# Kernel optimization log

Hardware: AMD Instinct MI355X
Metric: run time of the kernel (lower is better)

Reference implementation:

```python
import jax, jax.numpy as jnp
import numpy as np
from jax import lax

CHAR_H = 100
HIDDEN = 512
N_LABELS = 64
WORD_D = 300
CHAR_D = 50
FORGET_BIAS = 1.0
BN_EPS = 1e-3


def lstm(x, W, b, lens):
    """TF BasicLSTMCell dynamic_rnn. x:[B,T,D], W:[D+H,4H], b:[4H], lens:[B].
    Returns (outputs [B,T,H] zeroed past lens, (c,h) final states held at lens)."""
    B, T, _ = x.shape
    H = W.shape[1] // 4
    def step(carry, inp):
        c, h = carry
        xt, t = inp
        z = jnp.concatenate([xt, h], axis=-1) @ W + b
        i, j, f, o = jnp.split(z, 4, axis=-1)  # TF gate order i, j(g), f, o
        c_new = c * jax.nn.sigmoid(f + FORGET_BIAS) + jax.nn.sigmoid(i) * jnp.tanh(j)
        h_new = jnp.tanh(c_new) * jax.nn.sigmoid(o)
        active = (t < lens)[:, None]
        c = jnp.where(active, c_new, c)
        h = jnp.where(active, h_new, h)
        out = jnp.where(active, h_new, jnp.zeros_like(h_new))
        return (c, h), out
    init = (jnp.zeros((B, H), x.dtype), jnp.zeros((B, H), x.dtype))
    (c, h), outs = lax.scan(step, init, (jnp.swapaxes(x, 0, 1), jnp.arange(T)))
    return jnp.swapaxes(outs, 0, 1), (c, h)


def reverse_seq(x, lens):
    """tf.reverse_sequence along time axis 1."""
    T = x.shape[1]
    t = jnp.arange(T)[None, :]
    idx = jnp.where(t < lens[:, None], lens[:, None] - 1 - t, t)
    return jnp.take_along_axis(x, idx[:, :, None], axis=1)


def _glorot(key, shape):
    fan_in, fan_out = shape[0], shape[1]
    s = np.sqrt(6.0 / (fan_in + fan_out)).astype(np.float32)
    return jax.random.uniform(key, shape, jnp.float32, -s, s)


def setup_inputs() -> dict:
    key = jax.random.key(0)
    ks = jax.random.split(key, 16)
    N_SUB, SUB_T = 16384, 25
    B, T = 64, 256
    d_word_in = WORD_D + 2 * CHAR_H  # 500
    inp = {
        "subwords": jax.random.normal(ks[0], (N_SUB, SUB_T, CHAR_D), jnp.float32),
        "tokens": jax.random.normal(ks[1], (B, T, WORD_D), jnp.float32),
        "token_subword": jax.random.randint(ks[2], (B, T), 0, N_SUB, jnp.int32),
        "subword_seq_lens": jax.random.randint(ks[3], (N_SUB,), 1, SUB_T + 1, jnp.int32),
        "seq_lens": jax.random.randint(ks[4], (B,), 1, T + 1, jnp.int32),
        "Wc_f": _glorot(ks[5], (CHAR_D + CHAR_H, 4 * CHAR_H)),
        "bc_f": jnp.zeros((4 * CHAR_H,), jnp.float32),
        "Wc_b": _glorot(ks[6], (CHAR_D + CHAR_H, 4 * CHAR_H)),
        "bc_b": jnp.zeros((4 * CHAR_H,), jnp.float32),
        "Ww_f": _glorot(ks[7], (d_word_in + HIDDEN, 4 * HIDDEN)),
        "bw_f": jnp.zeros((4 * HIDDEN,), jnp.float32),
        "Ww_b": _glorot(ks[8], (d_word_in + HIDDEN, 4 * HIDDEN)),
        "bw_b": jnp.zeros((4 * HIDDEN,), jnp.float32),
        "Wo": _glorot(ks[9], (2 * HIDDEN + HIDDEN, 4 * HIDDEN)),
        "bo": jnp.zeros((4 * HIDDEN,), jnp.float32),
        "bn_gamma": jnp.ones((HIDDEN,), jnp.float32),
        "bn_beta": jnp.zeros((HIDDEN,), jnp.float32),
        "Wt": _glorot(ks[10], (HIDDEN, N_LABELS)),
        "bt": jnp.zeros((N_LABELS,), jnp.float32),
    }
    return inp


def reference(subwords, tokens, token_subword, subword_seq_lens, seq_lens,
              Wc_f, bc_f, Wc_b, bc_b, Ww_f, bw_f, Ww_b, bw_b,
              Wo, bo, bn_gamma, bn_beta, Wt, bt):
    # --- char/subword BiLSTM: only final hidden states are used ---
    _, (_, hf) = lstm(subwords, Wc_f, bc_f, subword_seq_lens)
    _, (_, hb) = lstm(reverse_seq(subwords, subword_seq_lens), Wc_b, bc_b, subword_seq_lens)
    subword_reprs = jnp.concatenate([hf, hb], axis=1)           # [N_sub, 200]
    tok_sub = subword_reprs[token_subword]                      # [B,T,200]
    word_in = jnp.concatenate([tokens, tok_sub], axis=2)        # [B,T,500]
    # --- word BiLSTM ---
    f_out, _ = lstm(word_in, Ww_f, bw_f, seq_lens)
    b_out_r, _ = lstm(reverse_seq(word_in, seq_lens), Ww_b, bw_b, seq_lens)
    b_out = reverse_seq(b_out_r, seq_lens)
    hidden = jnp.concatenate([f_out, b_out], axis=2)            # [B,T,1024]
    # --- top unidirectional LSTM ---
    out2, _ = lstm(hidden, Wo, bo, seq_lens)                    # [B,T,512]
    # --- batch norm over all but last dim (contrib.layers.batch_norm) ---
    mean = jnp.mean(out2, axis=(0, 1))
    var = jnp.var(out2, axis=(0, 1))
    bn = bn_gamma * (out2 - mean) * lax.rsqrt(var + BN_EPS) + bn_beta
    # --- tag affine ---
    logits = bn @ Wt + bt                                       # [B,T,n_labels]
    return logits
```

## Files before the change

### kernel.cpp

```cpp
#include <hip/hip_runtime.h>
#include <cstdint>
#include <cstddef>


typedef unsigned short bf_t;
typedef __attribute__((ext_vector_type(8))) short bf16x8;
typedef __attribute__((ext_vector_type(4))) float f32x4;

#define DEVI __device__ __forceinline__
DEVI float bf2f(bf_t u){ return __uint_as_float(((unsigned)u)<<16); }
DEVI bf_t  f2bf(float f){ unsigned u=__float_as_uint(f); return (bf_t)((u + 0x7FFFu + ((u>>16)&1u))>>16); }
DEVI float sigx(float x){ return __builtin_amdgcn_rcpf(1.0f + __builtin_amdgcn_exp2f(-1.44269504f*x)); }
DEVI float tanx(float x){ return 2.0f*__builtin_amdgcn_rcpf(1.0f + __builtin_amdgcn_exp2f(-2.88539008f*x)) - 1.0f; }

__global__ void k_dbg(float* out, unsigned mb){ out[0] = (float)mb; }

__global__ __launch_bounds__(256) void k_prep_charm(const float* __restrict__ wcf,
    const float* __restrict__ wcb, bf_t* __restrict__ wct){
  int i = blockIdx.x*256 + threadIdx.x;
  if (i >= 2*400*160) return;
  int kk = i % 160; int r = i / 160;
  int np = r % 400; int dir = r / 400;
  int u = np >> 2, g = np & 3;
  const float* w = dir ? wcb : wcf;
  wct[i] = (kk < 150) ? f2bf(w[kk*400 + g*100 + u]) : (bf_t)0;
}
__global__ __launch_bounds__(256) void k_prep_wrec(const float* __restrict__ wwf,
    const float* __restrict__ wwb, bf_t* __restrict__ wrg){
  int i = blockIdx.x*256 + threadIdx.x;
  if (i >= 2*2048*512) return;
  int k = i & 511; int np = (i >> 9) & 2047; int dir = i >> 20;
  int c = np >> 2, g = np & 3;
  const float* w = dir ? wwb : wwf;
  wrg[i] = f2bf(w[(size_t)(500 + k)*2048 + g*512 + c]);
}
__global__ __launch_bounds__(256) void k_prep_trec(const float* __restrict__ wo,
    bf_t* __restrict__ wog){
  int i = blockIdx.x*256 + threadIdx.x;
  if (i >= 2048*512) return;
  int k = i & 511; int np = i >> 9;
  int c = np >> 2, g = np & 3;
  wog[i] = f2bf(wo[(size_t)(1024 + k)*2048 + g*512 + c]);
}
__global__ __launch_bounds__(256) void k_prep_wx(const float* __restrict__ wwf,
    const float* __restrict__ wwb, bf_t* __restrict__ wx){
  int i = blockIdx.x*256 + threadIdx.x;
  if (i >= 2*2048*512) return;
  int k = i & 511; int r = i >> 9;
  int np = r & 2047; int dir = r >> 11;
  int c = np >> 2, g = np & 3;
  const float* w = dir ? wwb : wwf;
  wx[i] = (k < 500) ? f2bf(w[(size_t)k*2048 + g*512 + c]) : (bf_t)0;
}
__global__ __launch_bounds__(256) void k_prep_wxt(const float* __restrict__ wo,
    bf_t* __restrict__ wxt){
  int i = blockIdx.x*256 + threadIdx.x;
  if (i >= 2048*1024) return;
  int k = i & 1023; int np = i >> 10;
  int c = np >> 2, g = np & 3;
  wxt[i] = f2bf(wo[(size_t)k*2048 + g*512 + c]);
}
__global__ __launch_bounds__(256) void k_prep_bias(const float* __restrict__ bwf,
    const float* __restrict__ bwb, const float* __restrict__ bo,
    float* __restrict__ bpf, float* __restrict__ bpb, float* __restrict__ bpt){
  int np = blockIdx.x*256 + threadIdx.x;
  if (np >= 2048) return;
  int c = np >> 2, g = np & 3;
  bpf[np] = bwf[g*512 + c];
  bpb[np] = bwb[g*512 + c];
  bpt[np] = bo[g*512 + c];
}
__global__ __launch_bounds__(256) void k_ridx(const int* __restrict__ lens,
    int* __restrict__ ridxb){
  int b = blockIdx.x, t = threadIdx.x;
  int L = lens[b];
  int tin = (t < L) ? (L - 1 - t) : t;
  ridxb[b*256 + t] = b*256 + tin;
}

DEVI int aslot(int s, int kk){
  return (((kk >> 5)*4 + ((kk >> 3) & 3))*16 + s)*8 + (kk & 7);
}
__global__ __launch_bounds__(256) void k_charm(const float* __restrict__ subwords,
    const int* __restrict__ slens, const bf_t* __restrict__ wct,
    const float* __restrict__ bcf, const float* __restrict__ bcb,
    bf_t* __restrict__ rep){
  const int dir = blockIdx.y;
  const int s0 = blockIdx.x * 16;
  const int tid = threadIdx.x;
  const int w = tid >> 6, lane = tid & 63;
  const int l16 = lane & 15, lk = lane >> 4;

  __shared__ __align__(16) bf_t abuf[2560];
  __shared__ float zs[16][409];
  __shared__ float bs[400];
  __shared__ int lens[16];

  if (tid < 16) lens[tid] = slens[s0 + tid];
  for (int i = tid; i < 1280; i += 256) ((float*)abuf)[i] = 0.f;
  {
    const float* bc = dir ? bcb : bcf;
    for (int i = tid; i < 400; i += 256) bs[i] = bc[(i & 3)*100 + (i >> 2)];
  }
  __syncthreads();

  int si[4], ki[4], Lr[4]; bool vr[4];
#pragma unroll
  for (int r = 0; r < 4; r++) {
    int i = tid + r*256;
    vr[r] = (i < 800);
    si[r] = vr[r] ? (i / 50) : 0;
    ki[r] = vr[r] ? (i - si[r]*50) : 0;
    Lr[r] = lens[si[r]];
  }
  float pf[4];
  auto loadx = [&](int t){
#pragma unroll
    for (int r = 0; r < 4; r++) {
      if (vr[r]) {
        int te = dir ? (Lr[r] - 1 - t) : t;
        te = te < 0 ? 0 : te;
        pf[r] = subwords[((size_t)(s0 + si[r])*25 + te)*50 + ki[r]];
      }
    }
  };
  loadx(0);

  const bf_t* wctd = wct + (size_t)dir*400*160;
  float c7[7];
#pragma unroll
  for (int j = 0; j < 7; j++) c7[j] = 0.f;

  for (int t = 0; t < 25; t++) {
#pragma unroll
    for (int r = 0; r < 4; r++)
      if (vr[r]) abuf[aslot(si[r], ki[r])] = f2bf(pf[r]);
    __syncthreads();
    if (t < 24) loadx(t + 1);

    f32x4 acc[7];
#pragma unroll
    for (int jj = 0; jj < 7; jj++) acc[jj] = (f32x4){0.f,0.f,0.f,0.f};
#pragma unroll
    for (int ks = 0; ks < 5; ks++) {
      bf16x8 af = *(const bf16x8*)&abuf[((ks*4 + lk)*16 + l16)*8];
#pragma unroll
      for (int jj = 0; jj < 7; jj++) {
        int j = w + jj*4;
        if (j < 25) {
          bf16x8 bv = *(const bf16x8*)(wctd + (size_t)(j*16 + l16)*160 + ks*32 + lk*8);
          acc[jj] = __builtin_amdgcn_mfma_f32_16x16x32_bf16(af, bv, acc[jj], 0, 0, 0);
        }
      }
    }
#pragma unroll
    for (int jj = 0; jj < 7; jj++) {
      int j = w + jj*4;
      if (j < 25) {
#pragma unroll
        for (int r = 0; r < 4; r++)
          zs[lk*4 + r][j*16 + l16] = acc[jj][r];
      }
    }
    __syncthreads();

#pragma unroll
    for (int j = 0; j < 7; j++) {
      int idx = j*256 + tid;
      if (idx < 1600) {
        int s = idx & 15, u = idx >> 4;
        int L = lens[s];
        if (t < L) {
          float zi = zs[s][u*4 + 0] + bs[u*4 + 0];
          float zj = zs[s][u*4 + 1] + bs[u*4 + 1];
          float zf = zs[s][u*4 + 2] + bs[u*4 + 2];
          float zo = zs[s][u*4 + 3] + bs[u*4 + 3];
          float cn = c7[j]*sigx(zf + 1.0f) + sigx(zi)*tanx(zj);
          float hn = tanx(cn)*sigx(zo);
          c7[j] = cn;
          bf_t hb = f2bf(hn);
          abuf[aslot(s, 50 + u)] = hb;
          if (t == L - 1) rep[(size_t)(s0 + s)*200 + dir*100 + u] = hb;
        }
      }
    }
  }
}

__global__ __launch_bounds__(128) void k_win(const float* __restrict__ tokens,
    const bf_t* __restrict__ rep, const int* __restrict__ tsub,
    bf_t* __restrict__ win){
  int row = blockIdx.x;
  int idx = tsub[row];
  const float* tsrc = tokens + (size_t)row*300;
  const bf_t* rsrc = rep + (size_t)idx*200;
  bf_t* w = win + (size_t)row*512;
  for (int i = threadIdx.x; i < 512; i += 128)
    w[i] = (i < 300) ? f2bf(tsrc[i]) : (i < 500 ? rsrc[i - 300] : (bf_t)0);
}

__global__ __launch_bounds__(256) void k_mgemm(const bf_t* __restrict__ A, int lda, int K,
    const bf_t* __restrict__ B0, const bf_t* __restrict__ B1,
    const float* __restrict__ bp0, const float* __restrict__ bp1,
    bf_t* __restrict__ C0, bf_t* __restrict__ C1,
    const int* __restrict__ ridx1, int t0){
  const int z = blockIdx.z;
  const bf_t* B = z ? B1 : B0;
  const float* bp = z ? bp1 : bp0;
  bf_t* C = z ? C1 : C0;
  const int* ridx = z ? ridx1 : nullptr;
  __shared__ short As[4096];
  __shared__ short Bs[4096];
  const int tid = threadIdx.x;
  const int rb = blockIdx.y*128, nb = blockIdx.x*128;
  const bf_t* srcA[2]; const bf_t* srcB[2];
#pragma unroll
  for (int q = 0; q < 2; q++) {
    int s = tid + q*256;
    int row = ((s >> 6) << 4) + (s & 15), kg = (s >> 4) & 3;
    int lr = rb + row;
    int v = (t0 >= 0) ? ((lr >> 6)*256 + t0 + (lr & 63)) : lr;
    int ga = ridx ? ridx[v] : v;
    srcA[q] = A + (size_t)ga*lda + kg*8;
    srcB[q] = B + (size_t)(nb + row)*K + kg*8;
  }
  f32x4 acc[4][4];
#pragma unroll
  for (int i = 0; i < 4; i++)
#pragma unroll
    for (int j = 0; j < 4; j++) acc[i][j] = (f32x4){0.f,0.f,0.f,0.f};
  const int wid = tid >> 6, lane = tid & 63;
  const int wr = wid >> 1, wc = wid & 1;
  const int l16 = lane & 15, lk = lane >> 4;

  uint4 va0 = *(const uint4*)(srcA[0]);
  uint4 va1 = *(const uint4*)(srcA[1]);
  uint4 vb0 = *(const uint4*)(srcB[0]);
  uint4 vb1 = *(const uint4*)(srcB[1]);
  for (int kb = 0; kb < K; kb += 32) {
    __syncthreads();
    *(uint4*)&As[(size_t)tid*8] = va0;
    *(uint4*)&As[(size_t)(tid+256)*8] = va1;
    *(uint4*)&Bs[(size_t)tid*8] = vb0;
    *(uint4*)&Bs[(size_t)(tid+256)*8] = vb1;
    __syncthreads();
    if (kb + 32 < K) {
      va0 = *(const uint4*)(srcA[0] + kb + 32);
      va1 = *(const uint4*)(srcA[1] + kb + 32);
      vb0 = *(const uint4*)(srcB[0] + kb + 32);
      vb1 = *(const uint4*)(srcB[1] + kb + 32);
    }
    bf16x8 af[4], bfr[4];
#pragma unroll
    for (int f = 0; f < 4; f++) {
      af[f]  = *(const bf16x8*)&As[(((wr*4 + f)*4 + lk)*16 + l16)*8];
      bfr[f] = *(const bf16x8*)&Bs[(((wc*4 + f)*4 + lk)*16 + l16)*8];
    }
#pragma unroll
    for (int i = 0; i < 4; i++)
#pragma unroll
      for (int j = 0; j < 4; j++)
        acc[i][j] = __builtin_amdgcn_mfma_f32_16x16x32_bf16(af[i], bfr[j], acc[i][j], 0, 0, 0);
  }
#pragma unroll
  for (int i = 0; i < 4; i++) {
    int row0 = wr*64 + i*16 + lk*4;
#pragma unroll
    for (int j = 0; j < 4; j++) {
      int col = nb + wc*64 + j*16 + l16;
      float bv = bp[col];
#pragma unroll
      for (int r = 0; r < 4; r++)
        C[(size_t)(rb + row0 + r)*2048 + col] = f2bf(acc[i][j][r] + bv);
    }
  }
}

__global__ __launch_bounds__(512) void k_chunk(
    bf_t* __restrict__ hx0, bf_t* __restrict__ hx1,
    float* __restrict__ cst, const bf_t* __restrict__ wrec,
    const bf_t* __restrict__ zxf, const bf_t* __restrict__ zxb,
    const int* __restrict__ seq_lens, bf_t* __restrict__ outp,
    unsigned* __restrict__ ctrs, int t0, int is_top){
  const int dir = is_top ? 0 : blockIdx.y;
  const int n = blockIdx.x;
  const int npb = n*128;
  const unsigned nblk = gridDim.x;
  unsigned* ctr = ctrs + dir*32;
  const int tid = threadIdx.x;
  const int w = tid >> 6, lane = tid & 63;
  const int l16 = lane & 15, lk = lane >> 4;

  __shared__ __align__(16) char smem[65536];
  float (*zs)[132] = (float(*)[132])smem;

  const bf_t* B = wrec + ((size_t)dir*2048 + npb + w*16)*512;
  const bf_t* zx = (dir ? zxb : zxf);
  unsigned long long* hx08 = (unsigned long long*)hx0 + (size_t)dir*8192;
  unsigned long long* hx18 = (unsigned long long*)hx1 + (size_t)dir*8192;

  bf16x8 bfr[16];
#pragma unroll
  for (int ks = 0; ks < 16; ks++)
    bfr[ks] = *(const bf16x8*)(B + (size_t)l16*512 + ks*32 + lk*8);

  const int b = tid >> 3, q = tid & 7, u0 = q*4;
  const int len = seq_lens[b];
  const int cg0 = (npb >> 2) + u0;
  const size_t cbase = ((size_t)dir*64 + b)*512 + cg0;
  float creg[4];
#pragma unroll
  for (int it = 0; it < 4; it++) creg[it] = cst[cbase + it];
  const size_t hslot = (size_t)n*512 + b*8 + q;
  unsigned long long hpack = __hip_atomic_load(
      ((t0 & 1) ? hx18 : hx08) + hslot,
      __ATOMIC_RELAXED, __HIP_MEMORY_SCOPE_AGENT);

  for (int s = 0; s < 64; s++) {
    const int t = t0 + s;
    unsigned long long* hr8 = (t & 1) ? hx18 : hx08;
    unsigned long long* hw8 = (t & 1) ? hx08 : hx18;

    const int tl = t & 63;
    uint4 zq[2];
    {
      const char* zxp = (const char*)(zx + ((size_t)(b*64 + tl))*2048 + (size_t)(npb + u0*4));
      zq[0] = *(const uint4*)zxp;
      zq[1] = *(const uint4*)(zxp + 16);
    }

#pragma unroll
    for (int it = 0; it < 16; it++) {
      int i = it*512 + tid;
      int nn = i >> 9, r9 = i & 511;
      int bb = r9 >> 3, qq = r9 & 7;
      unsigned long long v = __hip_atomic_load(hr8 + i,
          __ATOMIC_RELAXED, __HIP_MEMORY_SCOPE_AGENT);
      int cb = nn*64 + qq*8;
      *(unsigned long long*)&smem[bb*1024 + (((cb & ~15) ^ ((bb & 7) << 4)) | (cb & 15))] = v;
    }
    __syncthreads();

    f32x4 acc[4];
#pragma unroll
    for (int mf = 0; mf < 4; mf++) acc[mf] = (f32x4){0.f,0.f,0.f,0.f};
#pragma unroll
    for (int ks = 0; ks < 16; ks++) {
#pragma unroll
      for (int mf = 0; mf < 4; mf++) {
        int row = mf*16 + l16;
        bf16x8 af = *(const bf16x8*)&smem[row*1024 + ((ks*64 + lk*16) ^ ((row & 7) << 4))];
        acc[mf] = __builtin_amdgcn_mfma_f32_16x16x32_bf16(af, bfr[ks], acc[mf], 0, 0, 0);
      }
    }
    __syncthreads();

#pragma unroll
    for (int mf = 0; mf < 4; mf++)
#pragma unroll
      for (int r = 0; r < 4; r++)
        zs[mf*16 + lk*4 + r][w*16 + l16] = acc[mf][r];
    __syncthreads();

    if (t < len) {
      const ushort* zu = (const ushort*)zq;
      bf_t hb4[4];
#pragma unroll
      for (int it = 0; it < 4; it++) {
        float zi = zs[b][(u0 + it)*4 + 0] + bf2f(zu[it*4 + 0]);
        float zj = zs[b][(u0 + it)*4 + 1] + bf2f(zu[it*4 + 1]);
        float zf = zs[b][(u0 + it)*4 + 2] + bf2f(zu[it*4 + 2]);
        float zo = zs[b][(u0 + it)*4 + 3] + bf2f(zu[it*4 + 3]);
        float cn = creg[it]*sigx(zf + 1.0f) + sigx(zi)*tanx(zj);
        float hn = tanx(cn)*sigx(zo);
        creg[it] = cn;
        hb4[it] = f2bf(hn);
      }
      hpack = *(unsigned long long*)hb4;
      if (is_top) {
        *(ushort4*)&outp[((size_t)b*256 + t)*512 + cg0] = *(ushort4*)hb4;
      } else {
        int tin = dir ? (len - 1 - t) : t;
        *(ushort4*)&outp[((size_t)b*256 + tin)*1024 + dir*512 + cg0] = *(ushort4*)hb4;
      }
    }
    __hip_atomic_store(hw8 + hslot, hpack,
                       __ATOMIC_RELAXED, __HIP_MEMORY_SCOPE_AGENT);

    __syncthreads();
    if (tid == 0) {
      __hip_atomic_fetch_add(ctr, 1u, __ATOMIC_RELAXED, __HIP_MEMORY_SCOPE_AGENT);
      unsigned tgt = (unsigned)(s + 1) * nblk;
      while (__hip_atomic_load(ctr, __ATOMIC_RELAXED, __HIP_MEMORY_SCOPE_AGENT) < tgt) {
        __builtin_amdgcn_s_sleep(1);
      }
    }
    __syncthreads();
  }
#pragma unroll
  for (int it = 0; it < 4; it++) cst[cbase + it] = creg[it];
}

__global__ __launch_bounds__(256) void k_gemm_tag(const bf_t* __restrict__ A, int lda, int K,
    const float* __restrict__ W, int ldw, const float* __restrict__ bias,
    float* __restrict__ C, int ldc){
  const int nb = blockIdx.x*64, rb = blockIdx.y*128;
  const int tid = threadIdx.x;
  const int tr = tid >> 4, tc = tid & 15;
  __shared__ float As[16][132];
  __shared__ float Bs[16][68];
  float acc[8][4];
#pragma unroll
  for (int i = 0; i < 8; i++)
#pragma unroll
    for (int j = 0; j < 4; j++) acc[i][j] = 0.f;
  const int ar = tid >> 1, ak = (tid & 1)*8;
  const int bk = tid >> 4, bn = (tid & 15)*4;
  const bf_t* arow = A + (size_t)(rb + ar)*lda;
  for (int kb = 0; kb < K; kb += 16) {
#pragma unroll
    for (int j = 0; j < 8; j++)
      As[ak + j][ar] = bf2f(arow[kb + ak + j]);
    const float* wp = W + (size_t)(kb + bk)*ldw + nb + bn;
    Bs[bk][bn] = wp[0]; Bs[bk][bn+1] = wp[1]; Bs[bk][bn+2] = wp[2]; Bs[bk][bn+3] = wp[3];
    __syncthreads();
#pragma unroll
    for (int kk = 0; kk < 16; kk++) {
      float4 a0 = *(const float4*)&As[kk][tr*8];
      float4 a1 = *(const float4*)&As[kk][tr*8 + 4];
      float4 bq = *(const float4*)&Bs[kk][tc*4];
      float av[8] = {a0.x,a0.y,a0.z,a0.w,a1.x,a1.y,a1.z,a1.w};
      float bv[4] = {bq.x,bq.y,bq.z,bq.w};
#pragma unroll
      for (int i = 0; i < 8; i++)
#pragma unroll
        for (int j = 0; j < 4; j++) acc[i][j] += av[i]*bv[j];
    }
    __syncthreads();
  }
  float4 bb = *(const float4*)&bias[nb + tc*4];
  float bias4[4] = {bb.x, bb.y, bb.z, bb.w};
#pragma unroll
  for (int i = 0; i < 8; i++) {
    size_t row = rb + tr*8 + i;
#pragma unroll
    for (int j = 0; j < 4; j++)
      C[row*(size_t)ldc + nb + tc*4 + j] = acc[i][j] + bias4[j];
  }
}

__global__ __launch_bounds__(512) void k_bnstats(const bf_t* __restrict__ out2,
    float* __restrict__ gsum, float* __restrict__ gsq){
  int c = threadIdx.x;
  int r0 = blockIdx.x*256;
  float s = 0.f, q = 0.f;
  for (int i = 0; i < 256; i++) {
    float v = bf2f(out2[(size_t)(r0 + i)*512 + c]);
    s += v; q += v*v;
  }
  atomicAdd(&gsum[c], s);
  atomicAdd(&gsq[c], q);
}

__global__ __launch_bounds__(512) void k_bnfin(const float* __restrict__ gsum,
    const float* __restrict__ gsq, const float* __restrict__ gamma,
    const float* __restrict__ beta, const float* __restrict__ wt,
    const float* __restrict__ bt, float* __restrict__ wtp, float* __restrict__ btp){
  __shared__ float a_s[512], d_s[512];
  int c = threadIdx.x;
  float mean = gsum[c] * (1.0f/16384.0f);
  float var  = gsq[c]  * (1.0f/16384.0f) - mean*mean;
  float a = gamma[c] * rsqrtf(var + 1e-3f);
  a_s[c] = a;
  d_s[c] = beta[c] - mean*a;
  __syncthreads();
  for (int i = c; i < 512*64; i += 512) wtp[i] = a_s[i >> 6] * wt[i];
  if (c < 64) {
    float acc = bt[c];
    for (int cc = 0; cc < 512; cc++) acc += d_s[cc] * wt[cc*64 + c];
    btp[c] = acc;
  }
}

extern "C" void kernel_launch(void* const* d_in, const int* in_sizes, int n_in,
                              void* d_out, int out_size, void* d_ws, size_t ws_size,
                              hipStream_t stream) {
  const float* subwords = (const float*)d_in[0];
  const float* tokens   = (const float*)d_in[1];
  const int*   tsub     = (const int*)d_in[2];
  const int*   sublens  = (const int*)d_in[3];
  const int*   seqlens  = (const int*)d_in[4];
  const float* wcf = (const float*)d_in[5];
  const float* bcf = (const float*)d_in[6];
  const float* wcb = (const float*)d_in[7];
  const float* bcb = (const float*)d_in[8];
  const float* wwf = (const float*)d_in[9];
  const float* bwf = (const float*)d_in[10];
  const float* wwb = (const float*)d_in[11];
  const float* bwb = (const float*)d_in[12];
  const float* wo  = (const float*)d_in[13];
  const float* bo  = (const float*)d_in[14];
  const float* gma = (const float*)d_in[15];
  const float* bta = (const float*)d_in[16];
  const float* wt  = (const float*)d_in[17];
  const float* btb = (const float*)d_in[18];
  float* out = (float*)d_out;

  char* ws = (char*)d_ws;
  size_t off = 0;
  auto alc = [&](size_t bytes) -> void* {
    void* p = ws + off;
    off += (bytes + 255) & ~(size_t)255;
    return p;
  };
  bf_t* REP   = (bf_t*)alc(16384ull*200*2);
  bf_t* WIN   = (bf_t*)alc(16384ull*512*2);
  int*  RIDXB = (int*) alc(16384ull*4);
  bf_t* ZXF   = (bf_t*)alc(4096ull*2048*2);
  bf_t* ZXB   = (bf_t*)alc(4096ull*2048*2);
  bf_t* HID   = (bf_t*)alc(16384ull*1024*2);
  const size_t STATB = 131072 + 131072 + 65536 + 65536 + 262144 + 131072
                     + 2048 + 2048 + 2048;
  char* STAT0 = (char*)alc(STATB);
  bf_t* HXW0 = (bf_t*)STAT0;
  bf_t* HXW1 = (bf_t*)(STAT0 + 131072);
  bf_t* HXT0 = (bf_t*)(STAT0 + 262144);
  bf_t* HXT1 = (bf_t*)(STAT0 + 327680);
  float* CSW = (float*)(STAT0 + 393216);
  float* CST = (float*)(STAT0 + 655360);
  float* GSUM = (float*)(STAT0 + 786432);
  float* GSQ  = (float*)(STAT0 + 788480);
  unsigned* CTRS = (unsigned*)(STAT0 + 790528);
  float* WTP  = (float*)alc(512ull*64*4);
  float* BTP  = (float*)alc(64*4);
  bf_t* WCT  = (bf_t*)alc(2ull*400*160*2);
  bf_t* WRG  = (bf_t*)alc(2ull*2048*512*2);
  bf_t* WOG  = (bf_t*)alc(2048ull*512*2);
  bf_t* WXG  = (bf_t*)alc(2ull*2048*512*2);
  bf_t* WXT  = (bf_t*)alc(2048ull*1024*2);
  float* BPF = (float*)alc(2048*4);
  float* BPB = (float*)alc(2048*4);
  float* BPT = (float*)alc(2048*4);
  bf_t* ZXT  = ZXF;
  bf_t* OUT2 = ZXB;
  if (off > ws_size) {
    k_dbg<<<1, 1, 0, stream>>>(out, (unsigned)(ws_size >> 20));
    return;
  }

  hipMemsetAsync(HID, 0, 16384ull*1024*2, stream);
  hipMemsetAsync(STAT0, 0, STATB, stream);

  k_prep_charm<<<500, 256, 0, stream>>>(wcf, wcb, WCT);
  k_prep_wrec<<<8192, 256, 0, stream>>>(wwf, wwb, WRG);
  k_prep_trec<<<4096, 256, 0, stream>>>(wo, WOG);
  k_prep_wx<<<8192, 256, 0, stream>>>(wwf, wwb, WXG);
  k_prep_wxt<<<8192, 256, 0, stream>>>(wo, WXT);
  k_prep_bias<<<8, 256, 0, stream>>>(bwf, bwb, bo, BPF, BPB, BPT);
  k_ridx<<<64, 256, 0, stream>>>(seqlens, RIDXB);

  k_charm<<<dim3(1024, 2), 256, 0, stream>>>(subwords, sublens, WCT, bcf, bcb, REP);
  k_win<<<16384, 128, 0, stream>>>(tokens, REP, tsub, WIN);

  for (int ch = 0; ch < 4; ch++) {
    k_mgemm<<<dim3(16, 32, 2), 256, 0, stream>>>(WIN, 512, 512,
        WXG, WXG + 2048ull*512, BPF, BPB, ZXF, ZXB, RIDXB, ch*64);
    k_chunk<<<dim3(16, 2), 512, 0, stream>>>(HXW0, HXW1, CSW, WRG, ZXF, ZXB,
                                             seqlens, HID, CTRS + ch*64, ch*64, 0);
  }

  hipMemsetAsync(OUT2, 0, 16384ull*512*2, stream);
  for (int ch = 0; ch < 4; ch++) {
    k_mgemm<<<dim3(16, 32, 1), 256, 0, stream>>>(HID, 1024, 1024,
        WXT, nullptr, BPT, nullptr, ZXT, nullptr, nullptr, ch*64);
    k_chunk<<<dim3(16, 1), 512, 0, stream>>>(HXT0, HXT1, CST, WOG, ZXT, nullptr,
                                             seqlens, OUT2, CTRS + 256 + ch*32, ch*64, 1);
  }

  k_bnstats<<<64, 512, 0, stream>>>(OUT2, GSUM, GSQ);
  k_bnfin<<<1, 512, 0, stream>>>(GSUM, GSQ, gma, bta, wt, btb, WTP, BTP);
  k_gemm_tag<<<dim3(1, 128, 1), 256, 0, stream>>>(OUT2, 512, 512, WTP, 64, BTP, out, 64);
}
```

Baseline: 5.014 ms.

## Keep char-LSTM weights in registers and loop over subword groups per block

```diff
diff --git a/kernel.cpp b/kernel.cpp
--- a/kernel.cpp
+++ b/kernel.cpp
@@ -81,12 +81,11 @@
 DEVI int aslot(int s, int kk){
   return (((kk >> 5)*4 + ((kk >> 3) & 3))*16 + s)*8 + (kk & 7);
 }
-__global__ __launch_bounds__(256) void k_charm(const float* __restrict__ subwords,
+__global__ __launch_bounds__(512) void k_charm(const float* __restrict__ subwords,
     const int* __restrict__ slens, const bf_t* __restrict__ wct,
     const float* __restrict__ bcf, const float* __restrict__ bcb,
     bf_t* __restrict__ rep){
   const int dir = blockIdx.y;
-  const int s0 = blockIdx.x * 16;
   const int tid = threadIdx.x;
   const int w = tid >> 6, lane = tid & 63;
   const int l16 = lane & 15, lk = lane >> 4;
@@ -96,94 +95,110 @@
   __shared__ float bs[400];
   __shared__ int lens[16];
 
-  if (tid < 16) lens[tid] = slens[s0 + tid];
-  for (int i = tid; i < 1280; i += 256) ((float*)abuf)[i] = 0.f;
   {
     const float* bc = dir ? bcb : bcf;
-    for (int i = tid; i < 400; i += 256) bs[i] = bc[(i & 3)*100 + (i >> 2)];
-  }
-  __syncthreads();
-
-  int si[4], ki[4], Lr[4]; bool vr[4];
-#pragma unroll
-  for (int r = 0; r < 4; r++) {
-    int i = tid + r*256;
+    for (int i = tid; i < 400; i += 512) bs[i] = bc[(i & 3)*100 + (i >> 2)];
+  }
+
+  const bf_t* wctd = wct + (size_t)dir*400*160;
+  int jt[4];
+  bf16x8 breg[4][5];
+#pragma unroll
+  for (int jj = 0; jj < 4; jj++) {
+    int j = w + jj*8; jt[jj] = j;
+    int js = (j < 25) ? j : 0;
+#pragma unroll
+    for (int ks = 0; ks < 5; ks++)
+      breg[jj][ks] = *(const bf16x8*)(wctd + (size_t)(js*16 + l16)*160 + ks*32 + lk*8);
+  }
+
+  int si[2], ki[2]; bool vr[2];
+#pragma unroll
+  for (int r = 0; r < 2; r++) {
+    int i = tid + r*512;
     vr[r] = (i < 800);
     si[r] = vr[r] ? (i / 50) : 0;
     ki[r] = vr[r] ? (i - si[r]*50) : 0;
-    Lr[r] = lens[si[r]];
-  }
-  float pf[4];
-  auto loadx = [&](int t){
-#pragma unroll
-    for (int r = 0; r < 4; r++) {
+  }
+
+  for (int g = 0; g < 8; g++) {
+    const int s0 = (blockIdx.x*8 + g)*16;
+    int Lr[2];
+#pragma unroll
+    for (int r = 0; r < 2; r++) Lr[r] = vr[r] ? slens[s0 + si[r]] : 1;
+    if (tid < 16) lens[tid] = slens[s0 + tid];
+    for (int i = tid; i < 1280; i += 512) ((float*)abuf)[i] = 0.f;
+    float c4[4] = {0.f, 0.f, 0.f, 0.f};
+    float pf[2];
+#pragma unroll
+    for (int r = 0; r < 2; r++) {
       if (vr[r]) {
-        int te = dir ? (Lr[r] - 1 - t) : t;
+        int te = dir ? (Lr[r] - 1) : 0;
         te = te < 0 ? 0 : te;
         pf[r] = subwords[((size_t)(s0 + si[r])*25 + te)*50 + ki[r]];
       }
     }
-  };
-  loadx(0);
-
-  const bf_t* wctd = wct + (size_t)dir*400*160;
-  float c7[7];
-#pragma unroll
-  for (int j = 0; j < 7; j++) c7[j] = 0.f;
-
-  for (int t = 0; t < 25; t++) {
-#pragma unroll
-    for (int r = 0; r < 4; r++)
-      if (vr[r]) abuf[aslot(si[r], ki[r])] = f2bf(pf[r]);
-    __syncthreads();
-    if (t < 24) loadx(t + 1);
-
-    f32x4 acc[7];
-#pragma unroll
-    for (int jj = 0; jj < 7; jj++) acc[jj] = (f32x4){0.f,0.f,0.f,0.f};
-#pragma unroll
-    for (int ks = 0; ks < 5; ks++) {
-      bf16x8 af = *(const bf16x8*)&abuf[((ks*4 + lk)*16 + l16)*8];
-#pragma unroll
-      for (int jj = 0; jj < 7; jj++) {
-        int j = w + jj*4;
-        if (j < 25) {
-          bf16x8 bv = *(const bf16x8*)(wctd + (size_t)(j*16 + l16)*160 + ks*32 + lk*8);
-          acc[jj] = __builtin_amdgcn_mfma_f32_16x16x32_bf16(af, bv, acc[jj], 0, 0, 0);
+    __syncthreads();
+
+    for (int t = 0; t < 25; t++) {
+#pragma unroll
+      for (int r = 0; r < 2; r++)
+        if (vr[r]) abuf[aslot(si[r], ki[r])] = f2bf(pf[r]);
+      __syncthreads();
+      if (t < 24) {
+#pragma unroll
+        for (int r = 0; r < 2; r++) {
+          if (vr[r]) {
+            int te = dir ? (Lr[r] - 2 - t) : (t + 1);
+            te = te < 0 ? 0 : te;
+            pf[r] = subwords[((size_t)(s0 + si[r])*25 + te)*50 + ki[r]];
+          }
         }
       }
-    }
-#pragma unroll
-    for (int jj = 0; jj < 7; jj++) {
-      int j = w + jj*4;
-      if (j < 25) {
-#pragma unroll
-        for (int r = 0; r < 4; r++)
-          zs[lk*4 + r][j*16 + l16] = acc[jj][r];
-      }
-    }
-    __syncthreads();
-
-#pragma unroll
-    for (int j = 0; j < 7; j++) {
-      int idx = j*256 + tid;
-      if (idx < 1600) {
-        int s = idx & 15, u = idx >> 4;
-        int L = lens[s];
-        if (t < L) {
-          float zi = zs[s][u*4 + 0] + bs[u*4 + 0];
-          float zj = zs[s][u*4 + 1] + bs[u*4 + 1];
-          float zf = zs[s][u*4 + 2] + bs[u*4 + 2];
-          float zo = zs[s][u*4 + 3] + bs[u*4 + 3];
-          float cn = c7[j]*sigx(zf + 1.0f) + sigx(zi)*tanx(zj);
-          float hn = tanx(cn)*sigx(zo);
-          c7[j] = cn;
-          bf_t hb = f2bf(hn);
-          abuf[aslot(s, 50 + u)] = hb;
-          if (t == L - 1) rep[(size_t)(s0 + s)*200 + dir*100 + u] = hb;
+
+      f32x4 acc[4];
+#pragma unroll
+      for (int jj = 0; jj < 4; jj++) acc[jj] = (f32x4){0.f,0.f,0.f,0.f};
+#pragma unroll
+      for (int ks = 0; ks < 5; ks++) {
+        bf16x8 af = *(const bf16x8*)&abuf[((ks*4 + lk)*16 + l16)*8];
+#pragma unroll
+        for (int jj = 0; jj < 4; jj++)
+          if (jt[jj] < 25)
+            acc[jj] = __builtin_amdgcn_mfma_f32_16x16x32_bf16(af, breg[jj][ks], acc[jj], 0, 0, 0);
+      }
+#pragma unroll
+      for (int jj = 0; jj < 4; jj++) {
+        if (jt[jj] < 25) {
+#pragma unroll
+          for (int r = 0; r < 4; r++)
+            zs[lk*4 + r][jt[jj]*16 + l16] = acc[jj][r];
         }
       }
-    }
+      __syncthreads();
+
+#pragma unroll
+      for (int jc = 0; jc < 4; jc++) {
+        int idx = jc*512 + tid;
+        if (idx < 1600) {
+          int s = idx & 15, u = idx >> 4;
+          int L = lens[s];
+          if (t < L) {
+            float zi = zs[s][u*4 + 0] + bs[u*4 + 0];
+            float zj = zs[s][u*4 + 1] + bs[u*4 + 1];
+            float zf = zs[s][u*4 + 2] + bs[u*4 + 2];
+            float zo = zs[s][u*4 + 3] + bs[u*4 + 3];
+            float cn = c4[jc]*sigx(zf + 1.0f) + sigx(zi)*tanx(zj);
+            float hn = tanx(cn)*sigx(zo);
+            c4[jc] = cn;
+            bf_t hb = f2bf(hn);
+            abuf[aslot(s, 50 + u)] = hb;
+            if (t == L - 1) rep[(size_t)(s0 + s)*200 + dir*100 + u] = hb;
+          }
+        }
+      }
+    }
+    __syncthreads();
   }
 }
 
@@ -559,7 +574,7 @@
   k_prep_bias<<<8, 256, 0, stream>>>(bwf, bwb, bo, BPF, BPB, BPT);
   k_ridx<<<64, 256, 0, stream>>>(seqlens, RIDXB);
 
-  k_charm<<<dim3(1024, 2), 256, 0, stream>>>(subwords, sublens, WCT, bcf, bcb, REP);
+  k_charm<<<dim3(128, 2), 512, 0, stream>>>(subwords, sublens, WCT, bcf, bcb, REP);
   k_win<<<16384, 128, 0, stream>>>(tokens, REP, tsub, WIN);
 
   for (int ch = 0; ch < 4; ch++) {
```

New measurement: 4.806 ms. -4.1%, faster.
